# Optimization experiments

Hardware: AMD Instinct MI355X
Metric: run time of the kernel (lower is better)

The kernel has to match this reference:

```python
import jax, jax.numpy as jnp
import numpy as np
import math

EMBED_DIM = 1024
NUM_HEADS = 16
D_K = EMBED_DIM // NUM_HEADS  # 64 qubits per head
BATCH, SEQ = 4, 2048


def setup_inputs() -> dict:
    key = jax.random.key(0)
    k_x, k_th, k_w, k_b = jax.random.split(key, 4)
    x = jax.random.normal(k_x, (BATCH, SEQ, EMBED_DIM), dtype=jnp.float32)
    # trainable RX angle per head per qubit (tq.RX has one param each)
    theta = jax.random.normal(k_th, (NUM_HEADS, D_K), dtype=jnp.float32)
    # out_linear
    lim = 1.0 / math.sqrt(EMBED_DIM)
    w_out = jax.random.uniform(k_w, (EMBED_DIM, EMBED_DIM), jnp.float32, -lim, lim)
    b_out = jax.random.uniform(k_b, (EMBED_DIM,), jnp.float32, -lim, lim)
    return {"x": x, "theta": theta, "w_out": w_out, "b_out": b_out}


def reference(x, theta, w_out, b_out):
    B, S, E = x.shape
    H, d_k = theta.shape
    # Quantum head: RX(x_i) then RX(theta_i) on |0>, measure PauliZ ->
    # <Z_i> = cos(x_i + theta_i). No entangling gates in the code path.
    ang = x.reshape(B, S, H, d_k) + theta  # broadcast [H,d_k]
    qkv = jnp.cos(ang).transpose(0, 2, 1, 3)  # [B,H,S,d_k]; Q == K == V
    scale = 1.0 / math.sqrt(d_k)
    scores = jnp.einsum('bhqd,bhkd->bhqk', qkv, qkv) * scale
    attn = jax.nn.softmax(scores, axis=-1)  # dropout is identity in eval
    out = jnp.einsum('bhqk,bhkd->bhqd', attn, qkv)
    out = out.transpose(0, 2, 1, 3).reshape(B, S, E)
    return out @ w_out.T + b_out
```

## Files before the change

kernel.cpp:

```cpp
#include <hip/hip_runtime.h>


#define B_  4
#define S_  2048
#define H_  16
#define D_  64
#define E_  1024
#define EXP2_SCALE 0.18033688011112043f

typedef unsigned short u16;
typedef unsigned int u32;
typedef __attribute__((ext_vector_type(8))) short short8;
typedef __attribute__((ext_vector_type(4))) float floatx4;

static __device__ __forceinline__ float bf2f(u16 v) {
    return __uint_as_float(((unsigned)v) << 16);
}
static __device__ __forceinline__ u16 f2bf(float f) {
    unsigned u = __float_as_uint(f);
    return (u16)((u + 0x7FFFu + ((u >> 16) & 1u)) >> 16);
}
static __device__ __forceinline__ u32 pack_bf16_trunc(float lo, float hi) {
    return __builtin_amdgcn_perm(__float_as_uint(hi), __float_as_uint(lo), 0x07060302u);
}
static __device__ __forceinline__ short8 scale8(short8 v) {
    short8 o;
#pragma unroll
    for (int i = 0; i < 8; i++)
        o[i] = (short)f2bf(bf2f((u16)v[i]) * EXP2_SCALE);
    return o;
}

__global__ __launch_bounds__(256) void prep_kernel(const float* __restrict__ x,
                                                   const float* __restrict__ theta,
                                                   const float* __restrict__ W,
                                                   u16* __restrict__ qkv,
                                                   u16* __restrict__ qkvT,
                                                   u16* __restrict__ Wb) {
    __shared__ __align__(16) u16 TQ[64][72];
    int blk = blockIdx.x;
    int tid = threadIdx.x;
    if (blk >= 2048) {
        int i = ((blk - 2048) * 256 + tid) * 4;
        float4 w = *(const float4*)(W + i);
        ushort4 o;
        o.x = f2bf(w.x); o.y = f2bf(w.y); o.z = f2bf(w.z); o.w = f2bf(w.w);
        *(ushort4*)(Wb + i) = o;
        return;
    }
    int stile = blk & 31;
    int bh    = blk >> 5;
    int b     = bh >> 4;
    int h     = bh & 15;
    int i     = tid >> 2;
    int d0    = (tid & 3) << 4;
    int s0    = stile << 6;
    int s     = s0 + i;

    const float* xp = x + ((size_t)(b * S_ + s)) * E_ + h * D_ + d0;
    const float* tp = theta + h * D_ + d0;

    u16 ov[16];
#pragma unroll
    for (int j = 0; j < 16; j += 4) {
        float4 xv = *(const float4*)(xp + j);
        float4 tv = *(const float4*)(tp + j);
        ov[j]     = f2bf(__cosf(xv.x + tv.x));
        ov[j + 1] = f2bf(__cosf(xv.y + tv.y));
        ov[j + 2] = f2bf(__cosf(xv.z + tv.z));
        ov[j + 3] = f2bf(__cosf(xv.w + tv.w));
    }

    u16* qp = qkv + ((size_t)bh * S_ + s) * D_ + d0;
    *(uint4*)qp       = *(uint4*)&ov[0];
    *(uint4*)(qp + 8) = *(uint4*)&ov[8];

#pragma unroll
    for (int j = 0; j < 16; j++) TQ[d0 + j][i] = ov[j];
    __syncthreads();

    int d  = tid >> 2;
    int j0 = (tid & 3) << 4;
    u16 tmp[16];
#pragma unroll
    for (int j = 0; j < 16; j++) tmp[j] = TQ[d][j0 + j];
    u16* qtp = qkvT + ((size_t)bh * D_ + d) * S_ + s0 + j0;
    *(uint4*)qtp       = *(uint4*)&tmp[0];
    *(uint4*)(qtp + 8) = *(uint4*)&tmp[8];
}

__global__ __launch_bounds__(256, 4) void attn_kernel(const u16* __restrict__ qkv,
                                                      const u16* __restrict__ qkvT,
                                                      u16* __restrict__ aout) {
    int blk  = blockIdx.x;
    int qt   = blk & 15;
    int bh   = blk >> 4;
    int b    = bh >> 4;
    int h    = bh & 15;
    int tid  = threadIdx.x;
    int wave = tid >> 6;
    int lane = tid & 63;
    int lq   = lane & 15;
    int lg   = lane >> 4;
    int r    = tid >> 2;
    int c0   = (tid & 3) << 4;

    __shared__ __align__(16) u16 Kt[64][72];
    __shared__ __align__(16) u16 Vt[64][72];
    __shared__ __align__(16) u16 Pb[4][32][72];

    const u16* base  = qkv  + (size_t)bh * S_ * D_;
    const u16* baseT = qkvT + (size_t)bh * D_ * S_;
    int s0 = qt * 128;

    short8 bq[2][2];
#pragma unroll
    for (int rf = 0; rf < 2; rf++) {
        const u16* qrow = base + (size_t)(s0 + wave * 32 + rf * 16 + lq) * D_ + lg * 8;
        bq[rf][0] = scale8(*(const short8*)qrow);
        bq[rf][1] = scale8(*(const short8*)(qrow + 32));
    }

    floatx4 oacc[2][4] = {{{0,0,0,0},{0,0,0,0},{0,0,0,0},{0,0,0,0}},
                          {{0,0,0,0},{0,0,0,0},{0,0,0,0},{0,0,0,0}}};
    float lsum[2] = {0.f, 0.f};

    for (int kt = 0; kt < S_ / 64; kt++) {
        __syncthreads();
        {
            const u16* p = base + (size_t)(kt * 64 + r) * D_ + c0;
            *(uint4*)&Kt[r][c0]     = *(const uint4*)p;
            *(uint4*)&Kt[r][c0 + 8] = *(const uint4*)(p + 8);
            const u16* p2 = baseT + (size_t)r * S_ + kt * 64 + c0;
            *(uint4*)&Vt[r][c0]     = *(const uint4*)p2;
            *(uint4*)&Vt[r][c0 + 8] = *(const uint4*)(p2 + 8);
        }
        __syncthreads();

        floatx4 sc[2][4];
#pragma unroll
        for (int t = 0; t < 4; t++) {
            short8 a0 = *(short8*)&Kt[t * 16 + lq][lg * 8];
            short8 a1 = *(short8*)&Kt[t * 16 + lq][32 + lg * 8];
#pragma unroll
            for (int rf = 0; rf < 2; rf++) {
                floatx4 acc = {0, 0, 0, 0};
                acc = __builtin_amdgcn_mfma_f32_16x16x32_bf16(a0, bq[rf][0], acc, 0, 0, 0);
                sc[rf][t] = __builtin_amdgcn_mfma_f32_16x16x32_bf16(a1, bq[rf][1], acc, 0, 0, 0);
            }
        }

#pragma unroll
        for (int rf = 0; rf < 2; rf++) {
#pragma unroll
            for (int t = 0; t < 4; t++) {
                float p0 = __builtin_amdgcn_exp2f(sc[rf][t][0]);
                float p1 = __builtin_amdgcn_exp2f(sc[rf][t][1]);
                float p2 = __builtin_amdgcn_exp2f(sc[rf][t][2]);
                float p3 = __builtin_amdgcn_exp2f(sc[rf][t][3]);
                lsum[rf] += (p0 + p1) + (p2 + p3);
                uint2 w;
                w.x = pack_bf16_trunc(p0, p1);
                w.y = pack_bf16_trunc(p2, p3);
                *(uint2*)&Pb[wave][rf * 16 + lq][t * 16 + lg * 4] = w;
            }
        }

        asm volatile("s_waitcnt lgkmcnt(0)" ::: "memory");

        short8 bp[2][2];
#pragma unroll
        for (int rf = 0; rf < 2; rf++) {
            bp[rf][0] = *(short8*)&Pb[wave][rf * 16 + lq][lg * 8];
            bp[rf][1] = *(short8*)&Pb[wave][rf * 16 + lq][32 + lg * 8];
        }
#pragma unroll
        for (int t = 0; t < 4; t++) {
            short8 av0 = *(short8*)&Vt[t * 16 + lq][lg * 8];
            short8 av1 = *(short8*)&Vt[t * 16 + lq][32 + lg * 8];
#pragma unroll
            for (int rf = 0; rf < 2; rf++) {
                oacc[rf][t] = __builtin_amdgcn_mfma_f32_16x16x32_bf16(av0, bp[rf][0], oacc[rf][t], 0, 0, 0);
                oacc[rf][t] = __builtin_amdgcn_mfma_f32_16x16x32_bf16(av1, bp[rf][1], oacc[rf][t], 0, 0, 0);
            }
        }
    }

#pragma unroll
    for (int rf = 0; rf < 2; rf++) {
        lsum[rf] += __shfl_xor(lsum[rf], 16);
        lsum[rf] += __shfl_xor(lsum[rf], 32);
    }
#pragma unroll
    for (int rf = 0; rf < 2; rf++) {
        float inv = 1.0f / fmaxf(lsum[rf], 1e-20f);
        int srow = s0 + wave * 32 + rf * 16 + lq;
        u16* arow = aout + ((size_t)(b * S_ + srow)) * E_ + h * D_;
#pragma unroll
        for (int t = 0; t < 4; t++)
#pragma unroll
            for (int rr = 0; rr < 4; rr++)
                arow[t * 16 + lg * 4 + rr] = f2bf(oacc[rf][t][rr] * inv);
    }
}

__global__ __launch_bounds__(256) void proj_kernel(const u16* __restrict__ A,
                                                   const u16* __restrict__ Wb,
                                                   const float* __restrict__ bias,
                                                   float* __restrict__ out) {
    int m0   = blockIdx.x * 128;
    int n0   = blockIdx.y * 128;
    int tid  = threadIdx.x;
    int wave = tid >> 6;
    int wm   = wave >> 1;
    int wn   = wave & 1;
    int lane = tid & 63;
    int lq   = lane & 15;
    int lg   = lane >> 4;
    int r    = tid >> 1;
    int c0   = (tid & 1) * 32;

    __shared__ __align__(16) u16 As[128][72];
    __shared__ __align__(16) u16 Bs[128][72];

    floatx4 acc[4][4];
#pragma unroll
    for (int i = 0; i < 4; i++)
#pragma unroll
        for (int j = 0; j < 4; j++) acc[i][j] = (floatx4){0, 0, 0, 0};

    for (int kc = 0; kc < E_; kc += 64) {
        __syncthreads();
        const u16* pa = A + (size_t)(m0 + r) * E_ + kc + c0;
        const u16* pw = Wb + (size_t)(n0 + r) * E_ + kc + c0;
#pragma unroll
        for (int j = 0; j < 4; j++) {
            *(uint4*)&As[r][c0 + j * 8] = *(const uint4*)(pa + j * 8);
            *(uint4*)&Bs[r][c0 + j * 8] = *(const uint4*)(pw + j * 8);
        }
        __syncthreads();

#pragma unroll
        for (int c = 0; c < 2; c++) {
            short8 af[4], bf[4];
#pragma unroll
            for (int i = 0; i < 4; i++)
                af[i] = *(short8*)&As[wm * 64 + i * 16 + lq][c * 32 + lg * 8];
#pragma unroll
            for (int j = 0; j < 4; j++)
                bf[j] = *(short8*)&Bs[wn * 64 + j * 16 + lq][c * 32 + lg * 8];
#pragma unroll
            for (int i = 0; i < 4; i++)
#pragma unroll
                for (int j = 0; j < 4; j++)
                    acc[i][j] = __builtin_amdgcn_mfma_f32_16x16x32_bf16(af[i], bf[j], acc[i][j], 0, 0, 0);
        }
    }

#pragma unroll
    for (int j = 0; j < 4; j++) {
        int nidx = n0 + wn * 64 + j * 16 + lq;
        float bv = bias[nidx];
#pragma unroll
        for (int i = 0; i < 4; i++) {
#pragma unroll
            for (int rr = 0; rr < 4; rr++) {
                int row = m0 + wm * 64 + i * 16 + lg * 4 + rr;
                out[(size_t)row * E_ + nidx] = acc[i][j][rr] + bv;
            }
        }
    }
}

extern "C" void kernel_launch(void* const* d_in, const int* in_sizes, int n_in,
                              void* d_out, int out_size, void* d_ws, size_t ws_size,
                              hipStream_t stream) {
    const float* x     = (const float*)d_in[0];
    const float* theta = (const float*)d_in[1];
    const float* w_out = (const float*)d_in[2];
    const float* b_out = (const float*)d_in[3];
    float* out = (float*)d_out;

    char* ws = (char*)d_ws;
    const size_t QKV_BYTES = (size_t)B_ * H_ * S_ * D_ * sizeof(u16);
    u16* qkv  = (u16*)ws;
    u16* qkvT = (u16*)(ws + QKV_BYTES);
    u16* aout = (u16*)(ws + 2 * QKV_BYTES);
    u16* wbf  = (u16*)ws;
    u16* wbf_safe = (u16*)(ws + 3 * QKV_BYTES);

    prep_kernel<<<3072, 256, 0, stream>>>(x, theta, w_out, qkv, qkvT, wbf_safe);
    attn_kernel<<<(B_ * H_) * (S_ / 128), 256, 0, stream>>>(qkv, qkvT, aout);
    dim3 pg(B_ * S_ / 128, E_ / 128);
    proj_kernel<<<pg, 256, 0, stream>>>(aout, wbf_safe, b_out, out);
    (void)wbf;
}
```

Measured before the change: 203.3 us.

## Prefetch next K/V tile into registers and use direct global-to-LDS loads in projection

The attention kernel now loads the next K/V tile from global memory into registers while the current tile is being computed, so global latency overlaps with MFMA work. The projection GEMM replaces register-staged global-to-shared copies with global_load_lds direct transfers into an unpadded shared layout. The unpadded 64-wide rows may cause LDS bank conflicts on the fragment reads, and the explicit vmcnt(0) wait still serializes each load stage. Workspace pointer naming is also cleaned up.

```diff
diff --git a/kernel.cpp b/kernel.cpp
--- a/kernel.cpp
+++ b/kernel.cpp
@@ -29,6 +29,12 @@
     for (int i = 0; i < 8; i++)
         o[i] = (short)f2bf(bf2f((u16)v[i]) * EXP2_SCALE);
     return o;
+}
+
+static __device__ __forceinline__ void gload_lds16(const u16* g, u16* l) {
+    __builtin_amdgcn_global_load_lds(
+        (const __attribute__((address_space(1))) u32*)g,
+        (__attribute__((address_space(3))) u32*)l, 16, 0, 0);
 }
 
 __global__ __launch_bounds__(256) void prep_kernel(const float* __restrict__ x,
@@ -125,17 +131,32 @@
                           {{0,0,0,0},{0,0,0,0},{0,0,0,0},{0,0,0,0}}};
     float lsum[2] = {0.f, 0.f};
 
+    uint4 k0, k1, v0, v1;
+    {
+        const u16* p = base + (size_t)r * D_ + c0;
+        k0 = *(const uint4*)p;
+        k1 = *(const uint4*)(p + 8);
+        const u16* p2 = baseT + (size_t)r * S_ + c0;
+        v0 = *(const uint4*)p2;
+        v1 = *(const uint4*)(p2 + 8);
+    }
+
     for (int kt = 0; kt < S_ / 64; kt++) {
         __syncthreads();
-        {
-            const u16* p = base + (size_t)(kt * 64 + r) * D_ + c0;
-            *(uint4*)&Kt[r][c0]     = *(const uint4*)p;
-            *(uint4*)&Kt[r][c0 + 8] = *(const uint4*)(p + 8);
-            const u16* p2 = baseT + (size_t)r * S_ + kt * 64 + c0;
-            *(uint4*)&Vt[r][c0]     = *(const uint4*)p2;
-            *(uint4*)&Vt[r][c0 + 8] = *(const uint4*)(p2 + 8);
-        }
+        *(uint4*)&Kt[r][c0]     = k0;
+        *(uint4*)&Kt[r][c0 + 8] = k1;
+        *(uint4*)&Vt[r][c0]     = v0;
+        *(uint4*)&Vt[r][c0 + 8] = v1;
         __syncthreads();
+
+        if (kt + 1 < S_ / 64) {
+            const u16* p = base + (size_t)((kt + 1) * 64 + r) * D_ + c0;
+            k0 = *(const uint4*)p;
+            k1 = *(const uint4*)(p + 8);
+            const u16* p2 = baseT + (size_t)r * S_ + (kt + 1) * 64 + c0;
+            v0 = *(const uint4*)p2;
+            v1 = *(const uint4*)(p2 + 8);
+        }
 
         floatx4 sc[2][4];
 #pragma unroll
@@ -217,11 +238,9 @@
     int lane = tid & 63;
     int lq   = lane & 15;
     int lg   = lane >> 4;
-    int r    = tid >> 1;
-    int c0   = (tid & 1) * 32;
-
-    __shared__ __align__(16) u16 As[128][72];
-    __shared__ __align__(16) u16 Bs[128][72];
+
+    __shared__ __align__(16) u16 As[128 * 64];
+    __shared__ __align__(16) u16 Bs[128 * 64];
 
     floatx4 acc[4][4];
 #pragma unroll
@@ -231,13 +250,15 @@
 
     for (int kc = 0; kc < E_; kc += 64) {
         __syncthreads();
-        const u16* pa = A + (size_t)(m0 + r) * E_ + kc + c0;
-        const u16* pw = Wb + (size_t)(n0 + r) * E_ + kc + c0;
-#pragma unroll
-        for (int j = 0; j < 4; j++) {
-            *(uint4*)&As[r][c0 + j * 8] = *(const uint4*)(pa + j * 8);
-            *(uint4*)&Bs[r][c0 + j * 8] = *(const uint4*)(pw + j * 8);
-        }
+#pragma unroll
+        for (int c = 0; c < 4; c++) {
+            int cb = (wave * 4 + c) * 64;
+            int ci = cb + lane;
+            int row = ci >> 3, col8 = ci & 7;
+            gload_lds16(A  + (size_t)(m0 + row) * E_ + kc + col8 * 8, &As[(size_t)cb * 8]);
+            gload_lds16(Wb + (size_t)(n0 + row) * E_ + kc + col8 * 8, &Bs[(size_t)cb * 8]);
+        }
+        asm volatile("s_waitcnt vmcnt(0)" ::: "memory");
         __syncthreads();
 
 #pragma unroll
@@ -245,10 +266,10 @@
             short8 af[4], bf[4];
 #pragma unroll
             for (int i = 0; i < 4; i++)
-                af[i] = *(short8*)&As[wm * 64 + i * 16 + lq][c * 32 + lg * 8];
+                af[i] = *(short8*)&As[(wm * 64 + i * 16 + lq) * 64 + c * 32 + lg * 8];
 #pragma unroll
             for (int j = 0; j < 4; j++)
-                bf[j] = *(short8*)&Bs[wn * 64 + j * 16 + lq][c * 32 + lg * 8];
+                bf[j] = *(short8*)&Bs[(wn * 64 + j * 16 + lq) * 64 + c * 32 + lg * 8];
 #pragma unroll
             for (int i = 0; i < 4; i++)
 #pragma unroll
@@ -286,12 +307,10 @@
     u16* qkv  = (u16*)ws;
     u16* qkvT = (u16*)(ws + QKV_BYTES);
     u16* aout = (u16*)(ws + 2 * QKV_BYTES);
-    u16* wbf  = (u16*)ws;
-    u16* wbf_safe = (u16*)(ws + 3 * QKV_BYTES);
-
-    prep_kernel<<<3072, 256, 0, stream>>>(x, theta, w_out, qkv, qkvT, wbf_safe);
+    u16* wbf  = (u16*)(ws + 3 * QKV_BYTES);
+
+    prep_kernel<<<3072, 256, 0, stream>>>(x, theta, w_out, qkv, qkvT, wbf);
     attn_kernel<<<(B_ * H_) * (S_ / 128), 256, 0, stream>>>(qkv, qkvT, aout);
     dim3 pg(B_ * S_ / 128, E_ / 128);
-    proj_kernel<<<pg, 256, 0, stream>>>(aout, wbf_safe, b_out, out);
-    (void)wbf;
-}
+    proj_kernel<<<pg, 256, 0, stream>>>(aout, wbf, b_out, out);
+}
```

Result: no change. 206.4 us (+1.5%).
